# Kernel tuning notes

Measured on AMD Instinct MI355X. Metric: run time of the kernel, lower is better.

## Reference

```python
import jax, jax.numpy as jnp
import numpy as np
import math


def _alibi_slopes(n_heads):
    def pow2_slopes(n):
        start = 2.0 ** (-2.0 ** (-(math.log2(n) - 3)))
        return [start * start ** i for i in range(n)]
    if math.log2(n_heads) % 1 == 0:
        return np.array(pow2_slopes(n_heads), dtype=np.float32)
    closest = 2 ** math.floor(math.log2(n_heads))
    base = pow2_slopes(closest)
    extra = pow2_slopes(2 * closest)[0::2][: n_heads - closest]
    return np.array(base + extra, dtype=np.float32)


def setup_inputs() -> dict:
    key = jax.random.key(0)
    ks = jax.random.split(key, 5)
    B, T, D = 2, 2048, 1024
    scale = 1.0 / math.sqrt(D)
    return {
        "x": jax.random.normal(ks[0], (B, T, D), dtype=jnp.float32),
        "Wq": jax.random.normal(ks[1], (D, D), dtype=jnp.float32) * scale,
        "Wk": jax.random.normal(ks[2], (D, D), dtype=jnp.float32) * scale,
        "Wv": jax.random.normal(ks[3], (D, D), dtype=jnp.float32) * scale,
        "Wo": jax.random.normal(ks[4], (D, D), dtype=jnp.float32) * scale,
        "window": 256,
    }


def reference(x, Wq, Wk, Wv, Wo, window):
    B, T, D = x.shape
    H = 16
    d_k = D // H

    def proj(W):
        # torch nn.Linear: y = x @ W.T ; then (B,T,H,dk) -> (B,H,T,dk)
        return (x @ W.T).reshape(B, T, H, d_k).transpose(0, 2, 1, 3)

    Q, K, V = proj(Wq), proj(Wk), proj(Wv)
    scores = jnp.einsum("bhtk,bhsk->bhts", Q, K) / math.sqrt(d_k)

    pos = jnp.arange(T)
    dist = jnp.abs(pos[None, :] - pos[:, None]).astype(jnp.float32)  # (T,T)
    slopes = jnp.asarray(_alibi_slopes(H))  # (H,)
    alibi = -slopes[:, None, None] * dist  # (H,T,T)
    win_mask = jnp.where(dist > window // 2, -jnp.inf, 0.0)  # (T,T)

    scores = scores + alibi[None] + win_mask[None, None]
    attn = jax.nn.softmax(scores, axis=-1)  # dropout=0.0 (eval)
    out = jnp.einsum("bhts,bhsd->bthd", attn, V).reshape(B, T, D)
    return out @ Wo.T, attn
```

## Files before the change

kernel.cpp:

```cpp
#include <hip/hip_runtime.h>
#include <hip/hip_bf16.h>


typedef __bf16 bf16x8 __attribute__((ext_vector_type(8)));
typedef float f32x4 __attribute__((ext_vector_type(4)));

__device__ __forceinline__ float bf2f(unsigned short u) {
    union { unsigned int i; float f; } v; v.i = ((unsigned int)u) << 16; return v.f;
}
__device__ __forceinline__ unsigned short f2bf(float f) {
    union { float f; unsigned int i; } v; v.f = f;
    unsigned int r = v.i + 0x7FFFu + ((v.i >> 16) & 1u);
    return (unsigned short)(r >> 16);
}

__global__ __launch_bounds__(256) void cast_kernel(const float* __restrict__ in,
                                                   unsigned short* __restrict__ out, int n) {
    int i = (blockIdx.x * 256 + threadIdx.x) * 4;
    if (i < n) {
        const float4 v = *(const float4*)(in + i);
        ushort4 o;
        o.x = f2bf(v.x); o.y = f2bf(v.y); o.z = f2bf(v.z); o.w = f2bf(v.w);
        *(ushort4*)(out + i) = o;
    }
}

__global__ __launch_bounds__(256) void cast_w4(const float* __restrict__ a,
                                               const float* __restrict__ b,
                                               const float* __restrict__ c,
                                               const float* __restrict__ d,
                                               unsigned short* __restrict__ out) {
    const float* srcs[4] = {a, b, c, d};
    const float* src = srcs[blockIdx.y];
    const int i = (blockIdx.x * 256 + threadIdx.x) * 4;
    const float4 v = *(const float4*)(src + i);
    ushort4 o;
    o.x = f2bf(v.x); o.y = f2bf(v.y); o.z = f2bf(v.z); o.w = f2bf(v.w);
    *(ushort4*)(out + (size_t)blockIdx.y * 1048576 + i) = o;
}

#define GLDS16(g, l) __builtin_amdgcn_global_load_lds(                      \
    (const __attribute__((address_space(1))) void*)(g),                     \
    (__attribute__((address_space(3))) void*)(l), 16, 0, 0)

__global__ __launch_bounds__(256) void gemm_bf16_nt(
    const unsigned short* __restrict__ A, const unsigned short* __restrict__ Bm,
    float* __restrict__ C, unsigned short* __restrict__ qkv,
    int M, int N, int K, int mode)
{
    __shared__ __align__(16) unsigned short As[128 * 32];
    __shared__ __align__(16) unsigned short Bs[128 * 32];

    const int tid  = threadIdx.x;
    const int lane = tid & 63, w = tid >> 6;
    const int bm = blockIdx.y * 128, bn = blockIdx.x * 128;

    const unsigned short* ga = A  + (size_t)(bm + w * 16 + (lane >> 2)) * K + (lane & 3) * 8;
    const unsigned short* gb = Bm + (size_t)(bn + w * 16 + (lane >> 2)) * K + (lane & 3) * 8;
    unsigned short* laA0 = &As[w * 512];
    unsigned short* laA1 = &As[2048 + w * 512];
    unsigned short* laB0 = &Bs[w * 512];
    unsigned short* laB1 = &Bs[2048 + w * 512];

    const int wr = w >> 1, wc = w & 1;
    const int fr = lane & 15, fq = lane >> 4;

    f32x4 acc[4][4] = {};

    for (int k0 = 0; k0 < K; k0 += 32) {
        GLDS16(ga + k0, laA0);
        GLDS16(ga + k0 + (size_t)64 * K, laA1);
        GLDS16(gb + k0, laB0);
        GLDS16(gb + k0 + (size_t)64 * K, laB1);
        __syncthreads();
        bf16x8 af[4], bfv[4];
#pragma unroll
        for (int i = 0; i < 4; ++i)
            af[i] = *(const bf16x8*)&As[(wr * 64 + i * 16 + fr) * 32 + fq * 8];
#pragma unroll
        for (int j = 0; j < 4; ++j)
            bfv[j] = *(const bf16x8*)&Bs[(wc * 64 + j * 16 + fr) * 32 + fq * 8];
#pragma unroll
        for (int i = 0; i < 4; ++i)
#pragma unroll
            for (int j = 0; j < 4; ++j)
                acc[i][j] = __builtin_amdgcn_mfma_f32_16x16x32_bf16(af[i], bfv[j], acc[i][j], 0, 0, 0);
        __syncthreads();
    }

#pragma unroll
    for (int i = 0; i < 4; ++i) {
#pragma unroll
        for (int j = 0; j < 4; ++j) {
            const int mb = bm + wr * 64 + i * 16 + fq * 4;
            const int n  = bn + wc * 64 + j * 16 + fr;
#pragma unroll
            for (int r = 0; r < 4; ++r) {
                const int m = mb + r;
                const float val = acc[i][j][r];
                if (mode == 0) {
                    C[(size_t)m * N + n] = val;
                } else {
                    const int which = n >> 10, hh = (n >> 6) & 15, dd = n & 63;
                    const int bb = m >> 11, tt = m & 2047;
                    size_t off;
                    if (which == 2)
                        off = (size_t)2 * 4194304 + (((size_t)bb * 16 + hh) * 64 + dd) * 2048 + tt;
                    else
                        off = (size_t)which * 4194304 + (((size_t)bb * 16 + hh) * 2048 + tt) * 64 + dd;
                    qkv[off] = f2bf(val);
                }
            }
        }
    }
}

#define NT_MAX 20
__global__ __launch_bounds__(256) void attn_mfma(
    const unsigned short* __restrict__ Q, const unsigned short* __restrict__ K,
    const unsigned short* __restrict__ VT, float* __restrict__ attn,
    unsigned short* __restrict__ ao, const int* __restrict__ wptr)
{
    const int T = 2048;
    __shared__ __align__(16) unsigned short Plds[4][16][328];

    const int bid = (int)blockIdx.x;
    const int swz = (bid & 7) * 128 + (bid >> 3);
    const int w = threadIdx.x >> 6, lane = threadIdx.x & 63;
    const int fr = lane & 15, fq = lane >> 4;

    const int tblk = swz & 31;
    const int h    = (swz >> 5) & 15;
    const int b    = swz >> 9;
    const int t0   = tblk * 64;

    const int W2 = wptr[0] >> 1;
    const int sA = (t0 - W2) > 0 ? (t0 - W2) : 0;
    int sB = t0 + 63 + W2; if (sB > T - 1) sB = T - 1;
    const int sEnd = sB + 1;
    const int nt  = (sEnd - sA) >> 4;
    const int ncc = (nt + 1) >> 1;

    const size_t bhT = ((size_t)b * 16 + h) * T;
    const unsigned short* Qbh  = Q  + bhT * 64;
    const unsigned short* Kbh  = K  + bhT * 64;
    const unsigned short* VTbh = VT + (((size_t)b * 16 + h) * 64) * T;

    bf16x8 aq0 = *(const bf16x8*)(Qbh + (size_t)(t0 + w * 16 + fr) * 64 + fq * 8);
    bf16x8 aq1 = *(const bf16x8*)(Qbh + (size_t)(t0 + w * 16 + fr) * 64 + 32 + fq * 8);

    const float slope = exp2f(-0.5f * (float)(h + 1));
    const int trow0 = t0 + w * 16 + fq * 4;

    f32x4 sc[NT_MAX];
#pragma unroll
    for (int st = 0; st < NT_MAX; ++st) {
        const int sbase = sA + st * 16;
        if (sbase < sEnd) {
            const unsigned short* kb = Kbh + (size_t)(sbase + fr) * 64 + fq * 8;
            bf16x8 b0 = *(const bf16x8*)(kb);
            bf16x8 b1 = *(const bf16x8*)(kb + 32);
            f32x4 sv = {0.f, 0.f, 0.f, 0.f};
            sv = __builtin_amdgcn_mfma_f32_16x16x32_bf16(aq0, b0, sv, 0, 0, 0);
            sv = __builtin_amdgcn_mfma_f32_16x16x32_bf16(aq1, b1, sv, 0, 0, 0);
            const int scol = sbase + fr;
#pragma unroll
            for (int rr = 0; rr < 4; ++rr) {
                const int d = trow0 + rr - scol;
                const int ad = d < 0 ? -d : d;
                const float val = sv[rr] * 0.125f - slope * (float)ad;
                sc[st][rr] = (ad <= W2) ? val : -1e30f;
            }
        } else {
            sc[st] = (f32x4){-1e30f, -1e30f, -1e30f, -1e30f};
        }
    }

    float inv[4];
#pragma unroll
    for (int rr = 0; rr < 4; ++rr) {
        float m = -1e30f;
#pragma unroll
        for (int st = 0; st < NT_MAX; ++st) m = fmaxf(m, sc[st][rr]);
#pragma unroll
        for (int off = 1; off < 16; off <<= 1) m = fmaxf(m, __shfl_xor(m, off, 64));
        float s = 0.f;
#pragma unroll
        for (int st = 0; st < NT_MAX; ++st) {
            const float p = __expf(sc[st][rr] - m);
            sc[st][rr] = p;
            s += p;
        }
#pragma unroll
        for (int off = 1; off < 16; off <<= 1) s += __shfl_xor(s, off, 64);
        inv[rr] = 1.0f / s;
    }

#pragma unroll
    for (int st = 0; st < NT_MAX; ++st) {
        const int sbase = sA + st * 16;
        if (sbase < sEnd) {
#pragma unroll
            for (int rr = 0; rr < 4; ++rr)
                Plds[w][fq * 4 + rr][st * 16 + fr] = f2bf(sc[st][rr] * inv[rr]);
        } else {
#pragma unroll
            for (int rr = 0; rr < 4; ++rr)
                Plds[w][fq * 4 + rr][st * 16 + fr] = 0;
        }
    }

    f32x4 oacc[4] = {};
    for (int c = 0; c < ncc; ++c) {
        const bf16x8 pa = *(const bf16x8*)&Plds[w][fr][c * 32 + fq * 8];
#pragma unroll
        for (int j = 0; j < 4; ++j) {
            const bf16x8 bv = *(const bf16x8*)(VTbh + (size_t)(j * 16 + fr) * T + sA + c * 32 + fq * 8);
            oacc[j] = __builtin_amdgcn_mfma_f32_16x16x32_bf16(pa, bv, oacc[j], 0, 0, 0);
        }
    }

    for (int i = 0; i < 16; ++i) {
        float* row = attn + (bhT + t0 + w * 16 + i) * T;
        const unsigned short* prow = &Plds[w][i][0];
#pragma unroll
        for (int it = 0; it < 8; ++it) {
            const int c = it * 256 + lane * 4;
            float4 v;
            if (c >= sA && c < sEnd) {
                const int pc = c - sA;
                v.x = bf2f(prow[pc + 0]);
                v.y = bf2f(prow[pc + 1]);
                v.z = bf2f(prow[pc + 2]);
                v.w = bf2f(prow[pc + 3]);
            } else {
                v.x = 0.f; v.y = 0.f; v.z = 0.f; v.w = 0.f;
            }
            *(float4*)(row + c) = v;
        }
    }

#pragma unroll
    for (int j = 0; j < 4; ++j)
#pragma unroll
        for (int rr = 0; rr < 4; ++rr)
            ao[((size_t)b * T + trow0 + rr) * 1024 + h * 64 + j * 16 + fr] = f2bf(oacc[j][rr]);
}

extern "C" void kernel_launch(void* const* d_in, const int* in_sizes, int n_in,
                              void* d_out, int out_size, void* d_ws, size_t ws_size,
                              hipStream_t stream)
{
    const float* x  = (const float*)d_in[0];
    const float* Wq = (const float*)d_in[1];
    const float* Wk = (const float*)d_in[2];
    const float* Wv = (const float*)d_in[3];
    const float* Wo = (const float*)d_in[4];
    const int*  win = (const int*)d_in[5];

    const int M = 4096, D = 1024;

    unsigned short* xb    = (unsigned short*)d_ws;
    unsigned short* Wqkvb = xb + (size_t)M * D;
    unsigned short* Wob   = Wqkvb + (size_t)3 * D * D;
    unsigned short* QKVb  = Wob + (size_t)D * D;
    unsigned short* AOb   = QKVb + (size_t)3 * M * D;

    float* out  = (float*)d_out;
    float* attn = out + (size_t)M * D;

    cast_kernel<<<M * D / 1024, 256, 0, stream>>>(x, xb, M * D);
    {
        dim3 g(D * D / 1024, 4);
        cast_w4<<<g, 256, 0, stream>>>(Wq, Wk, Wv, Wo, Wqkvb);
    }

    {
        dim3 g(3072 / 128, M / 128);
        gemm_bf16_nt<<<g, 256, 0, stream>>>(xb, Wqkvb, nullptr, QKVb, M, 3072, D, 1);
    }

    attn_mfma<<<1024, 256, 0, stream>>>(
        QKVb, QKVb + (size_t)M * D, QKVb + (size_t)2 * M * D, attn, AOb, win);

    {
        dim3 g(D / 128, M / 128);
        gemm_bf16_nt<<<g, 256, 0, stream>>>(AOb, Wob, out, nullptr, M, D, D, 0);
    }
}
```

Before: 221.3 us.

## Merge cast kernels and split attn zero-fill from window probability stores

Merges the x cast and the four weight casts into one launch, removing one kernel launch. In the attention kernel, the zero fill of the out-of-window part of each attn row now happens before the softmax, and the later store writes only the window columns. The P·V MFMA loop moves after the attn row stores. The intent is to overlap the large attn write traffic with compute and trim redundant branches, at the cost of a different store pattern.

```diff
diff --git a/kernel.cpp b/kernel.cpp
--- a/kernel.cpp
+++ b/kernel.cpp
@@ -14,29 +14,28 @@
     return (unsigned short)(r >> 16);
 }
 
-__global__ __launch_bounds__(256) void cast_kernel(const float* __restrict__ in,
-                                                   unsigned short* __restrict__ out, int n) {
-    int i = (blockIdx.x * 256 + threadIdx.x) * 4;
-    if (i < n) {
-        const float4 v = *(const float4*)(in + i);
-        ushort4 o;
-        o.x = f2bf(v.x); o.y = f2bf(v.y); o.z = f2bf(v.z); o.w = f2bf(v.w);
-        *(ushort4*)(out + i) = o;
-    }
-}
-
-__global__ __launch_bounds__(256) void cast_w4(const float* __restrict__ a,
-                                               const float* __restrict__ b,
-                                               const float* __restrict__ c,
-                                               const float* __restrict__ d,
-                                               unsigned short* __restrict__ out) {
-    const float* srcs[4] = {a, b, c, d};
-    const float* src = srcs[blockIdx.y];
+__global__ __launch_bounds__(256) void cast_all(
+    const float* __restrict__ x,
+    const float* __restrict__ wq, const float* __restrict__ wk,
+    const float* __restrict__ wv, const float* __restrict__ wo,
+    unsigned short* __restrict__ xb, unsigned short* __restrict__ wb)
+{
+    const int slice = blockIdx.y;
     const int i = (blockIdx.x * 256 + threadIdx.x) * 4;
+    const float* src;
+    unsigned short* dst;
+    if (slice < 4) {
+        src = x + (size_t)slice * 1048576;
+        dst = xb + (size_t)slice * 1048576;
+    } else {
+        const float* ws4[4] = {wq, wk, wv, wo};
+        src = ws4[slice - 4];
+        dst = wb + (size_t)(slice - 4) * 1048576;
+    }
     const float4 v = *(const float4*)(src + i);
     ushort4 o;
     o.x = f2bf(v.x); o.y = f2bf(v.y); o.z = f2bf(v.z); o.w = f2bf(v.w);
-    *(ushort4*)(out + (size_t)blockIdx.y * 1048576 + i) = o;
+    *(ushort4*)(dst + i) = o;
 }
 
 #define GLDS16(g, l) __builtin_amdgcn_global_load_lds(                      \
@@ -176,6 +175,15 @@
         }
     }
 
+    {
+        const float4 z4 = {0.f, 0.f, 0.f, 0.f};
+        for (int i = 0; i < 16; ++i) {
+            float* row = attn + (bhT + t0 + w * 16 + i) * T;
+            for (int c = lane * 4; c < sA; c += 256) *(float4*)(row + c) = z4;
+            for (int c = sEnd + lane * 4; c < T; c += 256) *(float4*)(row + c) = z4;
+        }
+    }
+
     float inv[4];
 #pragma unroll
     for (int rr = 0; rr < 4; ++rr) {
@@ -210,33 +218,31 @@
         }
     }
 
-    f32x4 oacc[4] = {};
-    for (int c = 0; c < ncc; ++c) {
-        const bf16x8 pa = *(const bf16x8*)&Plds[w][fr][c * 32 + fq * 8];
-#pragma unroll
-        for (int j = 0; j < 4; ++j) {
-            const bf16x8 bv = *(const bf16x8*)(VTbh + (size_t)(j * 16 + fr) * T + sA + c * 32 + fq * 8);
-            oacc[j] = __builtin_amdgcn_mfma_f32_16x16x32_bf16(pa, bv, oacc[j], 0, 0, 0);
-        }
-    }
-
     for (int i = 0; i < 16; ++i) {
         float* row = attn + (bhT + t0 + w * 16 + i) * T;
         const unsigned short* prow = &Plds[w][i][0];
 #pragma unroll
-        for (int it = 0; it < 8; ++it) {
-            const int c = it * 256 + lane * 4;
-            float4 v;
-            if (c >= sA && c < sEnd) {
-                const int pc = c - sA;
+        for (int jj = 0; jj < 2; ++jj) {
+            const int pc = (jj * 64 + lane) * 4;
+            const int c = sA + pc;
+            if (c < sEnd) {
+                float4 v;
                 v.x = bf2f(prow[pc + 0]);
                 v.y = bf2f(prow[pc + 1]);
                 v.z = bf2f(prow[pc + 2]);
                 v.w = bf2f(prow[pc + 3]);
-            } else {
-                v.x = 0.f; v.y = 0.f; v.z = 0.f; v.w = 0.f;
+                *(float4*)(row + c) = v;
             }
-            *(float4*)(row + c) = v;
+        }
+    }
+
+    f32x4 oacc[4] = {};
+    for (int c = 0; c < ncc; ++c) {
+        const bf16x8 pa = *(const bf16x8*)&Plds[w][fr][c * 32 + fq * 8];
+#pragma unroll
+        for (int j = 0; j < 4; ++j) {
+            const bf16x8 bv = *(const bf16x8*)(VTbh + (size_t)(j * 16 + fr) * T + sA + c * 32 + fq * 8);
+            oacc[j] = __builtin_amdgcn_mfma_f32_16x16x32_bf16(pa, bv, oacc[j], 0, 0, 0);
         }
     }
 
@@ -269,10 +275,9 @@
     float* out  = (float*)d_out;
     float* attn = out + (size_t)M * D;
 
-    cast_kernel<<<M * D / 1024, 256, 0, stream>>>(x, xb, M * D);
-    {
-        dim3 g(D * D / 1024, 4);
-        cast_w4<<<g, 256, 0, stream>>>(Wq, Wk, Wv, Wo, Wqkvb);
+    {
+        dim3 g(1024, 8);
+        cast_all<<<g, 256, 0, stream>>>(x, Wq, Wk, Wv, Wo, xb, Wqkvb);
     }
 
     {
```

Measured after the change: 217.6 us. About the same (-1.7%).
